# Optimization experiments

Hardware: AMD Instinct MI355X
Metric: run time of the kernel (lower is better)

Reference implementation:

```python
import jax, jax.numpy as jnp
import numpy as np

B, L, HID, NH = 2, 1024, 1024, 16
HEAD = HID // NH
BUCKETS = 256          # position_buckets -> pos_ebd_size = 256
MAX_POS = 512          # max_relative_positions
ATT_SPAN = BUCKETS     # att_span = pos_ebd_size
SCALE_FACTOR = 3       # 1 + c2p + p2c
EPS = 1e-7


def make_log_bucket_position(rel_pos, bucket_size, max_position):
    sign = jnp.sign(rel_pos)
    mid = bucket_size // 2
    abs_pos = jnp.where((rel_pos < mid) & (rel_pos > -mid), mid - 1, jnp.abs(rel_pos))
    log_pos = jnp.ceil(
        jnp.log(abs_pos.astype(jnp.float32) / mid)
        / np.float32(np.log((max_position - 1) / mid)) * (mid - 1)
    ) + mid
    return jnp.where(abs_pos <= mid, rel_pos.astype(jnp.float32),
                     log_pos * sign.astype(jnp.float32)).astype(jnp.int32)


def build_relative_position(q, k, bucket_size, max_position):
    rel = jnp.arange(q, dtype=jnp.int32)[:, None] - jnp.arange(k, dtype=jnp.int32)[None, :]
    rel = make_log_bucket_position(rel, bucket_size, max_position)
    return rel  # [q, k], values in [-att_span, att_span]


def setup_inputs() -> dict:
    key = jax.random.key(0)
    ks = jax.random.split(key, 12)
    s = 0.02
    return {
        "hidden_states": jax.random.normal(ks[0], (B, L, HID), jnp.float32),
        "attention_mask": jnp.ones((B, 1, L, L), jnp.int32),
        "rel_embeddings": jax.random.normal(ks[1], (2 * ATT_SPAN, HID), jnp.float32),
        "Wq": jax.random.normal(ks[2], (HID, HID), jnp.float32) * s,
        "bq": jnp.zeros((HID,), jnp.float32),
        "Wk": jax.random.normal(ks[3], (HID, HID), jnp.float32) * s,
        "bk": jnp.zeros((HID,), jnp.float32),
        "Wv": jax.random.normal(ks[4], (HID, HID), jnp.float32) * s,
        "bv": jnp.zeros((HID,), jnp.float32),
        "Wo": jax.random.normal(ks[5], (HID, HID), jnp.float32) * s,
        "bo": jnp.zeros((HID,), jnp.float32),
        "ln_gamma": jnp.ones((HID,), jnp.float32),
        "ln_beta": jnp.zeros((HID,), jnp.float32),
    }


def _heads(x):
    # [B, L, HID] -> [B, NH, L, HEAD]
    return x.reshape(x.shape[0], x.shape[1], NH, HEAD).transpose(0, 2, 1, 3)


def reference(hidden_states, attention_mask, rel_embeddings,
              Wq, bq, Wk, bk, Wv, bv, Wo, bo, ln_gamma, ln_beta):
    q = _heads(hidden_states @ Wq + bq)   # [B,NH,L,HEAD]
    k = _heads(hidden_states @ Wk + bk)
    v = _heads(hidden_states @ Wv + bv)

    scale = jnp.sqrt(jnp.float32(HEAD * SCALE_FACTOR))
    scores = jnp.einsum("bhqd,bhkd->bhqk", q, k) / scale  # [B,NH,L,L]

    # ---- disentangled attention bias (share_att_key=True) ----
    rel_pos = build_relative_position(L, L, BUCKETS, MAX_POS)  # [L,L]
    # pos projections reuse query/key projections (share_att_key)
    pos_key = (rel_embeddings @ Wk + bk).reshape(2 * ATT_SPAN, NH, HEAD).transpose(1, 0, 2)   # [NH,2S,HEAD]
    pos_query = (rel_embeddings @ Wq + bq).reshape(2 * ATT_SPAN, NH, HEAD).transpose(1, 0, 2)

    # c2p: content-to-position
    c2p_att = jnp.einsum("bhqd,hsd->bhqs", q, pos_key)                 # [B,NH,L,2S]
    c2p_pos = jnp.clip(rel_pos + ATT_SPAN, 0, 2 * ATT_SPAN - 1)        # [L,L]
    c2p_idx = jnp.broadcast_to(c2p_pos[None, None], (B, NH, L, L))
    c2p = jnp.take_along_axis(c2p_att, c2p_idx, axis=-1)               # [B,NH,L,L]

    # p2c: position-to-content
    p2c_att = jnp.einsum("bhkd,hsd->bhks", k, pos_query)               # [B,NH,L,2S]
    p2c_pos = jnp.clip(-rel_pos + ATT_SPAN, 0, 2 * ATT_SPAN - 1)       # [L,L]
    p2c_idx = jnp.broadcast_to(p2c_pos[None, None], (B, NH, L, L))
    p2c = jnp.take_along_axis(p2c_att, p2c_idx, axis=-1)               # [B,NH,K,Q]
    p2c = p2c.transpose(0, 1, 3, 2)                                    # [B,NH,Q,K]

    scores = scores + (c2p + p2c) / scale

    # ---- XSoftmax: masked softmax ----
    rmask = attention_mask == 0  # [B,1,L,L] broadcasts over heads
    logits = jnp.where(rmask, -jnp.inf, scores)
    probs = jax.nn.softmax(logits, axis=-1)
    probs = jnp.where(rmask, 0.0, probs)

    ctx = jnp.einsum("bhqk,bhkd->bhqd", probs, v)                      # [B,NH,L,HEAD]
    ctx = ctx.transpose(0, 2, 1, 3).reshape(B, L, HID)

    # ---- SelfOutput: dense + residual + LayerNorm ----
    out = ctx @ Wo + bo
    x = out + hidden_states
    mu = jnp.mean(x, axis=-1, keepdims=True)
    var = jnp.mean(jnp.square(x - mu), axis=-1, keepdims=True)
    return (x - mu) / jnp.sqrt(var + EPS) * ln_gamma + ln_beta
```

## Files before the change

kernel.cpp:

```cpp
#include <hip/hip_runtime.h>
#include <hip/hip_bf16.h>
#include <cstdint>
#include <cstddef>

typedef float f32x4 __attribute__((ext_vector_type(4)));
typedef short s16x8 __attribute__((ext_vector_type(8)));

#define OFF_IDX   0ull
#define OFF_XB    4096ull
#define OFF_WT    5246976ull
#define OFF_Q     13635584ull
#define OFF_K     17829888ull
#define OFF_VT    22024192ull
#define OFF_POSQ  26218496ull
#define OFF_POSK  27267072ull
#define OFF_MB    28315648ull
#define OFF_CTX   95424512ull
#define OFF_X     99618816ull

#define INV_SCALE 0.07216878364870322f

__device__ __forceinline__ short f2bf(float f) {
  unsigned u = __builtin_bit_cast(unsigned, f);
  unsigned r = (u + 0x7fffu + ((u >> 16) & 1u)) >> 16;
  return (short)r;
}
__device__ __forceinline__ float bf2f(short h) {
  unsigned u = ((unsigned)(unsigned short)h) << 16;
  return __builtin_bit_cast(float, u);
}

__global__ void build_idx(char* wsb) {
  int i = blockIdx.x * 256 + threadIdx.x;
  if (i >= 2047) return;
  int d = i - 1023;
  int ad = d < 0 ? -d : d;
  int bucket;
  if (ad <= 128) {
    bucket = d;
  } else {
    const float denom = 1.38433933f;
    float lp = ceilf(logf((float)ad * (1.0f / 128.0f)) / denom * 127.0f) + 128.0f;
    bucket = (int)lp * (d > 0 ? 1 : -1);
  }
  int idx = bucket + 256;
  idx = idx < 0 ? 0 : (idx > 511 ? 511 : idx);
  ((short*)(wsb + OFF_IDX))[i] = (short)idx;
}

__global__ __launch_bounds__(256) void build_maskbits(const int* __restrict__ mask,
                                                      char* __restrict__ wsb) {
  int word = blockIdx.x * 4 + (threadIdx.x >> 6);
  int lane = threadIdx.x & 63;
  int q = word & 1023, kt = (word >> 10) & 15, b = word >> 14;
  int mv = mask[((size_t)b * 1024 + q) * 1024 + kt * 64 + lane];
  unsigned long long bits = __ballot(mv != 0);
  if (lane == 0) ((unsigned long long*)(wsb + OFF_MB))[word] = bits;
}

__global__ __launch_bounds__(256) void convert_x(const float* __restrict__ hidden,
                                                 const float* __restrict__ rel,
                                                 char* __restrict__ wsb) {
  size_t gid = (size_t)blockIdx.x * 256 + threadIdx.x;
  const float* src = (gid < 524288) ? (hidden + gid * 4) : (rel + (gid - 524288) * 4);
  float4 v = *(const float4*)src;
  short* dst = (short*)(wsb + OFF_XB) + gid * 4;
  short4 o;
  o.x = f2bf(v.x); o.y = f2bf(v.y); o.z = f2bf(v.z); o.w = f2bf(v.w);
  *(short4*)dst = o;
}

__global__ __launch_bounds__(256) void transpose_w(const float* __restrict__ Wq,
                                                   const float* __restrict__ Wk,
                                                   const float* __restrict__ Wv,
                                                   const float* __restrict__ Wo,
                                                   char* __restrict__ wsb) {
  int z = blockIdx.z;
  const float* W = (z == 0) ? Wq : (z == 1) ? Wk : (z == 2) ? Wv : Wo;
  short* out = (short*)(wsb + OFF_WT) + (size_t)z * 1048576;
  int n0 = blockIdx.x * 32, k0 = blockIdx.y * 32;
  int tx = threadIdx.x & 31, ty = threadIdx.x >> 5;
  __shared__ float t[32][33];
#pragma unroll
  for (int i = 0; i < 4; ++i)
    t[ty + 8 * i][tx] = W[(size_t)(k0 + ty + 8 * i) * 1024 + n0 + tx];
  __syncthreads();
#pragma unroll
  for (int i = 0; i < 4; ++i)
    out[(size_t)(n0 + ty + 8 * i) * 1024 + k0 + tx] = f2bf(t[tx][ty + 8 * i]);
}

__global__ __launch_bounds__(256) void gemm_all(char* __restrict__ wsb, int mode,
    const float* __restrict__ bq, const float* __restrict__ bk, const float* __restrict__ bv,
    const float* __restrict__ bo, const float* __restrict__ hidden) {
  const int tid = threadIdx.x;
  const int w = tid >> 6, l = tid & 63;
  const int lr = l & 15, lg = l >> 4;
  const int wr = (w >> 1) * 64, wc = (w & 1) * 64;
  const int n0 = blockIdx.x * 128, m0 = blockIdx.y * 128;
  const int z = blockIdx.z;

  const short* A;
  const short* B;
  int lda, ldb, K;
  if (mode == 0) {
    if (z == 2 && m0 >= 2048) return;
    A = (const short*)(wsb + OFF_XB); lda = 1024;
    B = (const short*)(wsb + OFF_WT) + (size_t)z * 1048576; ldb = 1024;
    K = 1024;
  } else {
    A = (const short*)(wsb + OFF_CTX); lda = 1024;
    B = (const short*)(wsb + OFF_WT) + (size_t)3 * 1048576; ldb = 1024;
    K = 1024;
  }

  __shared__ __align__(16) short Al[128 * 32];
  __shared__ __align__(16) short Bl[128 * 32];

  f32x4 acc[4][4] = {};

  for (int k0 = 0; k0 < K; k0 += 32) {
#pragma unroll
    for (int j = 0; j < 2; ++j) {
      int c = w * 2 + j;
      int row = c * 16 + (l >> 2), col = (l & 3) * 8;
      const short* ga = A + (size_t)(m0 + row) * lda + k0 + col;
      const short* gb = B + (size_t)(n0 + row) * ldb + k0 + col;
      __builtin_amdgcn_global_load_lds((const __attribute__((address_space(1))) void*)ga,
          (__attribute__((address_space(3))) void*)(Al + c * 512), 16, 0, 0);
      __builtin_amdgcn_global_load_lds((const __attribute__((address_space(1))) void*)gb,
          (__attribute__((address_space(3))) void*)(Bl + c * 512), 16, 0, 0);
    }
    __syncthreads();
    s16x8 af[4], bfr[4];
#pragma unroll
    for (int i = 0; i < 4; ++i) af[i] = *(const s16x8*)&Al[(wr + i * 16 + lr) * 32 + lg * 8];
#pragma unroll
    for (int i = 0; i < 4; ++i) bfr[i] = *(const s16x8*)&Bl[(wc + i * 16 + lr) * 32 + lg * 8];
#pragma unroll
    for (int mi = 0; mi < 4; ++mi)
#pragma unroll
      for (int ni = 0; ni < 4; ++ni)
        acc[mi][ni] = __builtin_amdgcn_mfma_f32_16x16x32_bf16(af[mi], bfr[ni], acc[mi][ni], 0, 0, 0);
    __syncthreads();
  }

  if (mode == 0) {
    const float* bias = (z == 0) ? bq : (z == 1) ? bk : bv;
    short* outq = (short*)(wsb + ((z == 0) ? OFF_Q : (z == 1) ? OFF_K : OFF_VT));
    short* outp = (short*)(wsb + ((z == 0) ? OFF_POSQ : OFF_POSK));
#pragma unroll
    for (int mi = 0; mi < 4; ++mi) {
#pragma unroll
      for (int ni = 0; ni < 4; ++ni) {
        int gcol = n0 + wc + ni * 16 + lr;
        int h = gcol >> 6, d = gcol & 63;
        float bia = bias[gcol];
#pragma unroll
        for (int r = 0; r < 4; ++r) {
          int grow = m0 + wr + mi * 16 + lg * 4 + r;
          short v16 = f2bf(acc[mi][ni][r] + bia);
          if (z == 2) {
            int b = grow >> 10, ll = grow & 1023;
            outq[((size_t)((b * 16 + h) * 64 + d)) * 1024 + ll] = v16;
          } else if (grow < 2048) {
            int b = grow >> 10, ll = grow & 1023;
            outq[((size_t)((b * 16 + h) * 1024 + ll)) * 64 + d] = v16;
          } else {
            int s = grow - 2048;
            outp[((size_t)(h * 512 + s)) * 64 + d] = v16;
          }
        }
      }
    }
  } else {
    float* X = (float*)(wsb + OFF_X);
#pragma unroll
    for (int mi = 0; mi < 4; ++mi)
#pragma unroll
      for (int ni = 0; ni < 4; ++ni) {
        int gcol = n0 + wc + ni * 16 + lr;
        float bia = bo[gcol];
#pragma unroll
        for (int r = 0; r < 4; ++r) {
          int grow = m0 + wr + mi * 16 + lg * 4 + r;
          X[(size_t)grow * 1024 + gcol] =
              acc[mi][ni][r] + bia + hidden[(size_t)grow * 1024 + gcol];
        }
      }
  }
}

__global__ __launch_bounds__(256, 3) void attn_kernel(char* __restrict__ wsb) {
  const int bh = blockIdx.x, qt = blockIdx.y;
  const int b = bh >> 4, h = bh & 15;
  const int q0 = qt * 64;
  const int tid = threadIdx.x, w = tid >> 6, l = tid & 63;
  const int lr = l & 15, lg = l >> 4;

  const short* qb  = (const short*)(wsb + OFF_Q)  + (size_t)bh * 65536;
  const short* kb  = (const short*)(wsb + OFF_K)  + (size_t)bh * 65536;
  const short* vtb = (const short*)(wsb + OFF_VT) + (size_t)bh * 65536;
  const short* pkb = (const short*)(wsb + OFF_POSK) + (size_t)h * 32768;
  const short* pqb = (const short*)(wsb + OFF_POSQ) + (size_t)h * 32768;
  const short* idxg = (const short*)(wsb + OFF_IDX);
  const unsigned long long* mb =
      (const unsigned long long*)(wsb + OFF_MB) + (size_t)b * 16384;

  __shared__ __align__(16) short Kl[4096];
  __shared__ __align__(16) short Vl[4096];
  __shared__ __align__(16) short c2pw[4][16][104];
  __shared__ __align__(16) short p2cw[64][104];
  __shared__ __align__(16) short iiall[1088];

  for (int j = tid; j < 1087; j += 256) iiall[j] = idxg[q0 + j];

  s16x8 qf0, qf1;
  {
    int g = q0 + w * 16 + lr;
    const short* qp = qb + (size_t)g * 64 + lg * 8;
    qf0 = *(const s16x8*)qp;
    qf1 = *(const s16x8*)(qp + 32);
  }

  f32x4 acc[4] = {};
  float mrun[4] = {-1e30f, -1e30f, -1e30f, -1e30f};
  float lsum[4] = {0.f, 0.f, 0.f, 0.f};
  __syncthreads();

  for (int kt = 0; kt < 16; ++kt) {
    const int k0 = kt * 64;
    {
      int srow = tid >> 2, sc2 = (tid & 3) * 2, rx = srow & 7;
      const short* ks = kb + (size_t)(k0 + srow) * 64 + sc2 * 8;
      *(s16x8*)&Kl[srow * 64 + ((sc2 ^ rx) << 3)]       = *(const s16x8*)ks;
      *(s16x8*)&Kl[srow * 64 + (((sc2 + 1) ^ rx) << 3)] = *(const s16x8*)(ks + 8);
      const short* vs = vtb + (size_t)srow * 1024 + k0 + sc2 * 8;
      *(s16x8*)&Vl[srow * 64 + ((sc2 ^ rx) << 3)]       = *(const s16x8*)vs;
      *(s16x8*)&Vl[srow * 64 + (((sc2 + 1) ^ rx) << 3)] = *(const s16x8*)(vs + 8);
    }
    unsigned long long mw[4];
#pragma unroll
    for (int r = 0; r < 4; ++r)
      mw[r] = mb[(size_t)kt * 1024 + q0 + w * 16 + lg * 4 + r];
    __syncthreads();

    const int jbase = 960 - k0;
    const int loC  = iiall[w * 16 + jbase] & ~7;
    const int loPw = iiall[48 - w * 16 + jbase] & ~7;
    int loP[4];
#pragma unroll
    for (int cb = 0; cb < 4; ++cb) loP[cb] = iiall[48 - cb * 16 + jbase] & ~7;

    {
      f32x4 cacc[6] = {};
#pragma unroll
      for (int cb = 0; cb < 6; ++cb) {
        int i0 = loC + cb * 16 + lr;
        i0 = i0 > 511 ? 511 : i0;
        const short* bp = pkb + (size_t)i0 * 64 + lg * 8;
        s16x8 b0 = *(const s16x8*)bp;
        s16x8 b1 = *(const s16x8*)(bp + 32);
        cacc[cb] = __builtin_amdgcn_mfma_f32_16x16x32_bf16(qf0, b0, cacc[cb], 0, 0, 0);
        cacc[cb] = __builtin_amdgcn_mfma_f32_16x16x32_bf16(qf1, b1, cacc[cb], 0, 0, 0);
      }
#pragma unroll
      for (int cb = 0; cb < 6; ++cb)
#pragma unroll
        for (int r = 0; r < 4; ++r)
          c2pw[w][lg * 4 + r][cb * 16 + lr] = f2bf(cacc[cb][r]);
    }
    {
      int krow = w * 16 + lr, rx = krow & 7;
      s16x8 ka0 = *(const s16x8*)&Kl[krow * 64 + ((lg ^ rx) << 3)];
      s16x8 ka1 = *(const s16x8*)&Kl[krow * 64 + (((4 + lg) ^ rx) << 3)];
      f32x4 pacc[6] = {};
#pragma unroll
      for (int cb = 0; cb < 6; ++cb) {
        int i0 = loPw + cb * 16 + lr;
        i0 = i0 > 511 ? 511 : i0;
        const short* bp = pqb + (size_t)i0 * 64 + lg * 8;
        s16x8 b0 = *(const s16x8*)bp;
        s16x8 b1 = *(const s16x8*)(bp + 32);
        pacc[cb] = __builtin_amdgcn_mfma_f32_16x16x32_bf16(ka0, b0, pacc[cb], 0, 0, 0);
        pacc[cb] = __builtin_amdgcn_mfma_f32_16x16x32_bf16(ka1, b1, pacc[cb], 0, 0, 0);
      }
#pragma unroll
      for (int cb = 0; cb < 6; ++cb)
#pragma unroll
        for (int r = 0; r < 4; ++r)
          p2cw[w * 16 + lg * 4 + r][cb * 16 + lr] = f2bf(pacc[cb][r]);
    }
    f32x4 sf[4];
#pragma unroll
    for (int cb = 0; cb < 4; ++cb) {
      int krow = cb * 16 + lr, rx = krow & 7;
      s16x8 kf0 = *(const s16x8*)&Kl[krow * 64 + ((lg ^ rx) << 3)];
      s16x8 kf1 = *(const s16x8*)&Kl[krow * 64 + (((4 + lg) ^ rx) << 3)];
      f32x4 z4 = {};
      z4 = __builtin_amdgcn_mfma_f32_16x16x32_bf16(qf0, kf0, z4, 0, 0, 0);
      z4 = __builtin_amdgcn_mfma_f32_16x16x32_bf16(qf1, kf1, z4, 0, 0, 0);
      sf[cb] = z4;
    }
    __syncthreads();

    float pv[4][4];
    float tmax[4] = {-1e30f, -1e30f, -1e30f, -1e30f};
#pragma unroll
    for (int cb = 0; cb < 4; ++cb) {
      int colt = cb * 16 + lr;
#pragma unroll
      for (int r = 0; r < 4; ++r) {
        int rowl = lg * 4 + r;
        int jj = (w * 16 + rowl) - colt + 1023 - k0;
        int i = iiall[jj];
        float bias = bf2f(c2pw[w][rowl][i - loC]) + bf2f(p2cw[colt][i - loP[cb]]);
        float sv = (sf[cb][r] + bias) * INV_SCALE;
        bool ok = (mw[r] >> colt) & 1ull;
        sv = ok ? sv : -1e30f;
        pv[cb][r] = sv;
        tmax[r] = fmaxf(tmax[r], sv);
      }
    }
#pragma unroll
    for (int off = 1; off < 16; off <<= 1)
#pragma unroll
      for (int r = 0; r < 4; ++r) tmax[r] = fmaxf(tmax[r], __shfl_xor(tmax[r], off));
    float alpha[4];
#pragma unroll
    for (int r = 0; r < 4; ++r) {
      float mn = fmaxf(mrun[r], tmax[r]);
      alpha[r] = __expf(mrun[r] - mn);
      mrun[r] = mn;
    }
    float rsum[4] = {0.f, 0.f, 0.f, 0.f};
#pragma unroll
    for (int cb = 0; cb < 4; ++cb)
#pragma unroll
      for (int r = 0; r < 4; ++r) {
        float p = __expf(pv[cb][r] - mrun[r]);
        pv[cb][r] = p;
        rsum[r] += p;
      }
#pragma unroll
    for (int off = 1; off < 16; off <<= 1)
#pragma unroll
      for (int r = 0; r < 4; ++r) rsum[r] += __shfl_xor(rsum[r], off);
#pragma unroll
    for (int r = 0; r < 4; ++r) lsum[r] = lsum[r] * alpha[r] + rsum[r];
#pragma unroll
    for (int d2 = 0; d2 < 4; ++d2)
#pragma unroll
      for (int r = 0; r < 4; ++r) acc[d2][r] *= alpha[r];

#pragma unroll
    for (int cb = 0; cb < 4; ++cb)
#pragma unroll
      for (int r = 0; r < 4; ++r)
        c2pw[w][lg * 4 + r][cb * 16 + lr] = f2bf(pv[cb][r]);

    s16x8 pa0 = *(const s16x8*)&c2pw[w][lr][lg * 8];
    s16x8 pa1 = *(const s16x8*)&c2pw[w][lr][32 + lg * 8];
#pragma unroll
    for (int d2 = 0; d2 < 4; ++d2) {
      int drow = d2 * 16 + lr, rx = drow & 7;
      s16x8 vf0 = *(const s16x8*)&Vl[drow * 64 + ((lg ^ rx) << 3)];
      s16x8 vf1 = *(const s16x8*)&Vl[drow * 64 + (((4 + lg) ^ rx) << 3)];
      acc[d2] = __builtin_amdgcn_mfma_f32_16x16x32_bf16(pa0, vf0, acc[d2], 0, 0, 0);
      acc[d2] = __builtin_amdgcn_mfma_f32_16x16x32_bf16(pa1, vf1, acc[d2], 0, 0, 0);
    }
    __syncthreads();
  }

  short* ctx = (short*)(wsb + OFF_CTX);
#pragma unroll
  for (int r = 0; r < 4; ++r) {
    float inv = 1.0f / lsum[r];
    int gq = q0 + w * 16 + lg * 4 + r;
#pragma unroll
    for (int d2 = 0; d2 < 4; ++d2) {
      int gd = h * 64 + d2 * 16 + lr;
      ctx[((size_t)b * 1024 + gq) * 1024 + gd] = f2bf(acc[d2][r] * inv);
    }
  }
}

__global__ __launch_bounds__(256) void ln_kernel(const char* __restrict__ wsb,
                                                 const float* __restrict__ gamma,
                                                 const float* __restrict__ beta,
                                                 float* __restrict__ out) {
  int row = blockIdx.x, tid = threadIdx.x;
  const float* x = (const float*)(wsb + OFF_X) + (size_t)row * 1024;
  float4 v = ((const float4*)x)[tid];
  float s = v.x + v.y + v.z + v.w;
  float s2 = v.x * v.x + v.y * v.y + v.z * v.z + v.w * v.w;
#pragma unroll
  for (int off = 1; off < 64; off <<= 1) {
    s += __shfl_xor(s, off);
    s2 += __shfl_xor(s2, off);
  }
  __shared__ float ss[4], ss2[4];
  if ((tid & 63) == 0) { ss[tid >> 6] = s; ss2[tid >> 6] = s2; }
  __syncthreads();
  s = ss[0] + ss[1] + ss[2] + ss[3];
  s2 = ss2[0] + ss2[1] + ss2[2] + ss2[3];
  float mu = s * (1.0f / 1024.0f);
  float var = s2 * (1.0f / 1024.0f) - mu * mu;
  float rstd = rsqrtf(var + 1e-7f);
  float4 g = ((const float4*)gamma)[tid];
  float4 be = ((const float4*)beta)[tid];
  float4 o;
  o.x = (v.x - mu) * rstd * g.x + be.x;
  o.y = (v.y - mu) * rstd * g.y + be.y;
  o.z = (v.z - mu) * rstd * g.z + be.z;
  o.w = (v.w - mu) * rstd * g.w + be.w;
  ((float4*)(out + (size_t)row * 1024))[tid] = o;
}

extern "C" void kernel_launch(void* const* d_in, const int* in_sizes, int n_in,
                              void* d_out, int out_size, void* d_ws, size_t ws_size,
                              hipStream_t stream) {
  const float* hidden = (const float*)d_in[0];
  const int*   mask   = (const int*)d_in[1];
  const float* rel    = (const float*)d_in[2];
  const float* Wq = (const float*)d_in[3];
  const float* bq = (const float*)d_in[4];
  const float* Wk = (const float*)d_in[5];
  const float* bk = (const float*)d_in[6];
  const float* Wv = (const float*)d_in[7];
  const float* bv = (const float*)d_in[8];
  const float* Wo = (const float*)d_in[9];
  const float* bo = (const float*)d_in[10];
  const float* gamma = (const float*)d_in[11];
  const float* beta  = (const float*)d_in[12];
  char* ws = (char*)d_ws;
  float* out = (float*)d_out;

  build_idx<<<dim3(8), dim3(256), 0, stream>>>(ws);
  build_maskbits<<<dim3(8192), dim3(256), 0, stream>>>(mask, ws);
  convert_x<<<dim3(2560), dim3(256), 0, stream>>>(hidden, rel, ws);
  transpose_w<<<dim3(32, 32, 4), dim3(256), 0, stream>>>(Wq, Wk, Wv, Wo, ws);
  gemm_all<<<dim3(8, 20, 3), dim3(256), 0, stream>>>(ws, 0, bq, bk, bv, bo, hidden);
  attn_kernel<<<dim3(32, 16), dim3(256), 0, stream>>>(ws);
  gemm_all<<<dim3(8, 16, 1), dim3(256), 0, stream>>>(ws, 2, bq, bk, bv, bo, hidden);
  ln_kernel<<<dim3(2048), dim3(256), 0, stream>>>(ws, gamma, beta, out);
}
```

Before: 298.8 us.

## Split attention over key halves with flash-decode combine and direct global K/V loads

Splits each attention block's key range into two halves launched as separate blocks. The partial accumulators and running max/sum are written to workspace, and a new combine kernel merges them into ctx. This doubles the grid (512 to 1024 blocks), which helps fill the GPU's CUs. K and V tiles are no longer staged in shared memory; fragments are read straight from global memory, which drops a sync and raises occupancy to 4. The cost is an extra kernel launch, fp32 partial traffic, and possibly uncoalesced or redundant global reads of K and V.

```diff
diff --git a/kernel.cpp b/kernel.cpp
--- a/kernel.cpp
+++ b/kernel.cpp
@@ -15,6 +15,8 @@
 #define OFF_POSQ  26218496ull
 #define OFF_POSK  27267072ull
 #define OFF_MB    28315648ull
+#define OFF_PACC  28577792ull
+#define OFF_PML   45355008ull
 #define OFF_CTX   95424512ull
 #define OFF_X     99618816ull
 
@@ -191,8 +193,8 @@
   }
 }
 
-__global__ __launch_bounds__(256, 3) void attn_kernel(char* __restrict__ wsb) {
-  const int bh = blockIdx.x, qt = blockIdx.y;
+__global__ __launch_bounds__(256, 4) void attn_kernel(char* __restrict__ wsb) {
+  const int bh = blockIdx.x, qt = blockIdx.y, half = blockIdx.z;
   const int b = bh >> 4, h = bh & 15;
   const int q0 = qt * 64;
   const int tid = threadIdx.x, w = tid >> 6, l = tid & 63;
@@ -207,11 +209,9 @@
   const unsigned long long* mb =
       (const unsigned long long*)(wsb + OFF_MB) + (size_t)b * 16384;
 
-  __shared__ __align__(16) short Kl[4096];
-  __shared__ __align__(16) short Vl[4096];
   __shared__ __align__(16) short c2pw[4][16][104];
   __shared__ __align__(16) short p2cw[64][104];
-  __shared__ __align__(16) short iiall[1088];
+  __shared__ short iiall[1088];
 
   for (int j = tid; j < 1087; j += 256) iiall[j] = idxg[q0 + j];
 
@@ -228,29 +228,18 @@
   float lsum[4] = {0.f, 0.f, 0.f, 0.f};
   __syncthreads();
 
-  for (int kt = 0; kt < 16; ++kt) {
+  for (int kt = half * 8; kt < half * 8 + 8; ++kt) {
     const int k0 = kt * 64;
-    {
-      int srow = tid >> 2, sc2 = (tid & 3) * 2, rx = srow & 7;
-      const short* ks = kb + (size_t)(k0 + srow) * 64 + sc2 * 8;
-      *(s16x8*)&Kl[srow * 64 + ((sc2 ^ rx) << 3)]       = *(const s16x8*)ks;
-      *(s16x8*)&Kl[srow * 64 + (((sc2 + 1) ^ rx) << 3)] = *(const s16x8*)(ks + 8);
-      const short* vs = vtb + (size_t)srow * 1024 + k0 + sc2 * 8;
-      *(s16x8*)&Vl[srow * 64 + ((sc2 ^ rx) << 3)]       = *(const s16x8*)vs;
-      *(s16x8*)&Vl[srow * 64 + (((sc2 + 1) ^ rx) << 3)] = *(const s16x8*)(vs + 8);
-    }
+    const int jbase = 960 - k0;
+    const int loC  = iiall[w * 16 + jbase] & ~7;
+    int loP[4];
+#pragma unroll
+    for (int cb = 0; cb < 4; ++cb) loP[cb] = iiall[48 - cb * 16 + jbase] & ~7;
+
     unsigned long long mw[4];
 #pragma unroll
     for (int r = 0; r < 4; ++r)
       mw[r] = mb[(size_t)kt * 1024 + q0 + w * 16 + lg * 4 + r];
-    __syncthreads();
-
-    const int jbase = 960 - k0;
-    const int loC  = iiall[w * 16 + jbase] & ~7;
-    const int loPw = iiall[48 - w * 16 + jbase] & ~7;
-    int loP[4];
-#pragma unroll
-    for (int cb = 0; cb < 4; ++cb) loP[cb] = iiall[48 - cb * 16 + jbase] & ~7;
 
     {
       f32x4 cacc[6] = {};
@@ -271,10 +260,11 @@
           c2pw[w][lg * 4 + r][cb * 16 + lr] = f2bf(cacc[cb][r]);
     }
     {
-      int krow = w * 16 + lr, rx = krow & 7;
-      s16x8 ka0 = *(const s16x8*)&Kl[krow * 64 + ((lg ^ rx) << 3)];
-      s16x8 ka1 = *(const s16x8*)&Kl[krow * 64 + (((4 + lg) ^ rx) << 3)];
+      const short* kp = kb + (size_t)(k0 + w * 16 + lr) * 64 + lg * 8;
+      s16x8 ka0 = *(const s16x8*)kp;
+      s16x8 ka1 = *(const s16x8*)(kp + 32);
       f32x4 pacc[6] = {};
+      int loPw = loP[w];
 #pragma unroll
       for (int cb = 0; cb < 6; ++cb) {
         int i0 = loPw + cb * 16 + lr;
@@ -294,9 +284,9 @@
     f32x4 sf[4];
 #pragma unroll
     for (int cb = 0; cb < 4; ++cb) {
-      int krow = cb * 16 + lr, rx = krow & 7;
-      s16x8 kf0 = *(const s16x8*)&Kl[krow * 64 + ((lg ^ rx) << 3)];
-      s16x8 kf1 = *(const s16x8*)&Kl[krow * 64 + (((4 + lg) ^ rx) << 3)];
+      const short* kp = kb + (size_t)(k0 + cb * 16 + lr) * 64 + lg * 8;
+      s16x8 kf0 = *(const s16x8*)kp;
+      s16x8 kf1 = *(const s16x8*)(kp + 32);
       f32x4 z4 = {};
       z4 = __builtin_amdgcn_mfma_f32_16x16x32_bf16(qf0, kf0, z4, 0, 0, 0);
       z4 = __builtin_amdgcn_mfma_f32_16x16x32_bf16(qf1, kf1, z4, 0, 0, 0);
@@ -322,6 +312,8 @@
         tmax[r] = fmaxf(tmax[r], sv);
       }
     }
+    __syncthreads();
+
 #pragma unroll
     for (int off = 1; off < 16; off <<= 1)
 #pragma unroll
@@ -363,25 +355,54 @@
     s16x8 pa1 = *(const s16x8*)&c2pw[w][lr][32 + lg * 8];
 #pragma unroll
     for (int d2 = 0; d2 < 4; ++d2) {
-      int drow = d2 * 16 + lr, rx = drow & 7;
-      s16x8 vf0 = *(const s16x8*)&Vl[drow * 64 + ((lg ^ rx) << 3)];
-      s16x8 vf1 = *(const s16x8*)&Vl[drow * 64 + (((4 + lg) ^ rx) << 3)];
+      const short* vp = vtb + (size_t)(d2 * 16 + lr) * 1024 + k0 + lg * 8;
+      s16x8 vf0 = *(const s16x8*)vp;
+      s16x8 vf1 = *(const s16x8*)(vp + 32);
       acc[d2] = __builtin_amdgcn_mfma_f32_16x16x32_bf16(pa0, vf0, acc[d2], 0, 0, 0);
       acc[d2] = __builtin_amdgcn_mfma_f32_16x16x32_bf16(pa1, vf1, acc[d2], 0, 0, 0);
     }
-    __syncthreads();
-  }
-
-  short* ctx = (short*)(wsb + OFF_CTX);
+  }
+
+  const int part = (bh * 16 + qt) * 2 + half;
+  float* po = (float*)(wsb + OFF_PACC) + (size_t)part * 4096;
+  float* pml = (float*)(wsb + OFF_PML) + (size_t)part * 128;
 #pragma unroll
   for (int r = 0; r < 4; ++r) {
-    float inv = 1.0f / lsum[r];
-    int gq = q0 + w * 16 + lg * 4 + r;
-#pragma unroll
-    for (int d2 = 0; d2 < 4; ++d2) {
-      int gd = h * 64 + d2 * 16 + lr;
-      ctx[((size_t)b * 1024 + gq) * 1024 + gd] = f2bf(acc[d2][r] * inv);
-    }
+    int row = w * 16 + lg * 4 + r;
+#pragma unroll
+    for (int d2 = 0; d2 < 4; ++d2)
+      po[row * 64 + d2 * 16 + lr] = acc[d2][r];
+    if (lr == 0) { pml[row * 2] = mrun[r]; pml[row * 2 + 1] = lsum[r]; }
+  }
+}
+
+__global__ __launch_bounds__(256) void attn_combine(char* __restrict__ wsb) {
+  const int bh = blockIdx.x, qt = blockIdx.y;
+  const int b = bh >> 4, h = bh & 15, q0 = qt * 64;
+  const int tid = threadIdx.x;
+  const int q = tid >> 2, dc = (tid & 3) * 16;
+  const int p0 = (bh * 16 + qt) * 2, p1 = p0 + 1;
+  const float* a0 = (const float*)(wsb + OFF_PACC) + (size_t)p0 * 4096 + q * 64 + dc;
+  const float* a1 = (const float*)(wsb + OFF_PACC) + (size_t)p1 * 4096 + q * 64 + dc;
+  const float* ml0 = (const float*)(wsb + OFF_PML) + (size_t)p0 * 128 + q * 2;
+  const float* ml1 = (const float*)(wsb + OFF_PML) + (size_t)p1 * 128 + q * 2;
+  float m0 = ml0[0], l0 = ml0[1], m1 = ml1[0], l1 = ml1[1];
+  float m = fmaxf(m0, m1);
+  float w0 = __expf(m0 - m), w1 = __expf(m1 - m);
+  float lt = l0 * w0 + l1 * w1;
+  float inv = lt > 0.f ? 1.f / lt : 0.f;
+  w0 *= inv; w1 *= inv;
+  short* ctx = (short*)(wsb + OFF_CTX) + ((size_t)b * 1024 + q0 + q) * 1024 + h * 64 + dc;
+#pragma unroll
+  for (int j = 0; j < 16; j += 4) {
+    float4 x0 = *(const float4*)(a0 + j);
+    float4 x1 = *(const float4*)(a1 + j);
+    short4 o;
+    o.x = f2bf(x0.x * w0 + x1.x * w1);
+    o.y = f2bf(x0.y * w0 + x1.y * w1);
+    o.z = f2bf(x0.z * w0 + x1.z * w1);
+    o.w = f2bf(x0.w * w0 + x1.w * w1);
+    *(short4*)(ctx + j) = o;
   }
 }
 
@@ -441,7 +462,8 @@
   convert_x<<<dim3(2560), dim3(256), 0, stream>>>(hidden, rel, ws);
   transpose_w<<<dim3(32, 32, 4), dim3(256), 0, stream>>>(Wq, Wk, Wv, Wo, ws);
   gemm_all<<<dim3(8, 20, 3), dim3(256), 0, stream>>>(ws, 0, bq, bk, bv, bo, hidden);
-  attn_kernel<<<dim3(32, 16), dim3(256), 0, stream>>>(ws);
+  attn_kernel<<<dim3(32, 16, 2), dim3(256), 0, stream>>>(ws);
+  attn_combine<<<dim3(32, 16), dim3(256), 0, stream>>>(ws);
   gemm_all<<<dim3(8, 16, 1), dim3(256), 0, stream>>>(ws, 2, bq, bk, bv, bo, hidden);
   ln_kernel<<<dim3(2048), dim3(256), 0, stream>>>(ws, gamma, beta, out);
 }
```

New measurement: 329.4 us. 10.2% more time.
